# Performance work log

Measured on AMD Instinct MI355X. Metric: run time of the kernel, lower is better.

## Reference

```python
import jax, jax.numpy as jnp
import numpy as np

C, N = 3, 8192
FEATS = (64, 64, 1)
REG2, REG, REG_LENGTH = 1.0, 1.0, 4.0


def setup_inputs() -> dict:
    key = jax.random.key(0)
    k_x, k1, k2, k3 = jax.random.split(key, 4)
    x = jax.random.normal(k_x, (C, N), dtype=jnp.float32)
    # lecun_normal (flax Dense default): std = 1/sqrt(fan_in), no bias
    W1 = jax.random.normal(k1, (N, FEATS[0]), dtype=jnp.float32) / np.sqrt(N)
    W2 = jax.random.normal(k2, (FEATS[0], FEATS[1]), dtype=jnp.float32) / np.sqrt(FEATS[0])
    W3 = jax.random.normal(k3, (FEATS[1], FEATS[2]), dtype=jnp.float32) / np.sqrt(FEATS[1])
    regu2 = jnp.float32(REG2)
    regu = jnp.float32(REG)
    regu_length = jnp.float32(REG_LENGTH)
    return {"x": x, "W1": W1, "W2": W2, "W3": W3,
            "regu2": regu2, "regu": regu, "regu_length": regu_length}


def reference(x, W1, W2, W3, regu2, regu, regu_length):
    # x: (C, N)
    n = x.shape[1]
    # Circular cross-correlation rows: corr[i, j] = sum_c x[c, (i+j) % N] * x[c, i]
    corr = jax.vmap(
        lambda i: jnp.sum(jnp.roll(x, -i, axis=1) * x[:, i][:, None], axis=0)
    )(jnp.arange(n))  # (N, N)
    # tiny per-row MLP (Dense no-bias + elu), then sum over features
    z = jax.nn.elu(corr @ W1)
    z = jax.nn.elu(z @ W2)
    z = jax.nn.elu(z @ W3)
    per_row = jnp.sum(z, axis=-1)  # (N,)
    x2 = jnp.sum(x * x, axis=0)    # (N,)
    out = (jnp.mean(per_row)
           - regu2 * jnp.sum(x2)
           - regu * jnp.sum(jnp.exp(x2 / (2.0 * regu_length ** 2))))
    return out
```

## Files before the change

kernel.cpp:

```cpp
#include <hip/hip_runtime.h>
#include <hip/hip_bf16.h>

#define NN 8192
#define BM 32
#define BK 256
#define NT (NN / BK)
#define XWF 304

typedef short bfrag8 __attribute__((ext_vector_type(8)));
typedef float floatx4 __attribute__((ext_vector_type(4)));

static __device__ __forceinline__ unsigned short f2bf(float f) {
  unsigned u = __builtin_bit_cast(unsigned, f);
  u = (u + 0x7FFFu + ((u >> 16) & 1u)) >> 16;
  return (unsigned short)u;
}
static __device__ __forceinline__ unsigned cvt_pk_bf16(float a, float b) {
  return (unsigned)f2bf(a) | ((unsigned)f2bf(b) << 16);
}
static __device__ __forceinline__ float elu(float v) {
  return v > 0.f ? v : expm1f(v);
}

__global__ void prep_kernel(const float* __restrict__ x, const float* __restrict__ W1,
                            const float* __restrict__ W2, const float* __restrict__ rlen,
                            unsigned short* __restrict__ W1T, unsigned short* __restrict__ W2T,
                            float* __restrict__ acc) {
  const int b = blockIdx.x, t = threadIdx.x;
  if (b < 128) {
    __shared__ float tile[64][65];
    const int k0 = b * 64;
#pragma unroll
    for (int it = 0; it < 16; ++it) {
      int k = it * 4 + (t >> 6);
      tile[k][t & 63] = W1[(k0 + k) * 64 + (t & 63)];
    }
    __syncthreads();
#pragma unroll
    for (int it = 0; it < 16; ++it) {
      int f = it * 4 + (t >> 6);
      int kk = t & 63;
      W1T[f * NN + k0 + kk] = f2bf(tile[kk][f]);
    }
  } else if (b == 128) {
    for (int idx = t; idx < 64 * 64; idx += 256) {
      int k = idx >> 6, f = idx & 63;
      W2T[f * 64 + k] = f2bf(W2[idx]);
    }
  } else {
    float rl = rlen[0];
    float inv = 1.f / (2.f * rl * rl);
    int base = (b - 129) * 4096;
    float s1 = 0.f, s2 = 0.f;
    for (int ii = 0; ii < 16; ++ii) {
      int i = base + ii * 256 + t;
      float a0 = x[i], a1 = x[NN + i], a2 = x[2 * NN + i];
      float s = a0 * a0 + a1 * a1 + a2 * a2;
      s1 += s; s2 += expf(s * inv);
    }
    for (int d = 32; d > 0; d >>= 1) { s1 += __shfl_down(s1, d); s2 += __shfl_down(s2, d); }
    __shared__ float p1[4], p2[4];
    if ((t & 63) == 0) { p1[t >> 6] = s1; p2[t >> 6] = s2; }
    __syncthreads();
    if (t == 0) {
      atomicAdd(&acc[1], p1[0] + p1[1] + p1[2] + p1[3]);
      atomicAdd(&acc[2], p2[0] + p2[1] + p2[2] + p2[3]);
    }
  }
}

__global__ __launch_bounds__(512, 1) void main_kernel(
    const float* __restrict__ x, const unsigned short* __restrict__ W1T,
    const unsigned short* __restrict__ W2T, const float* __restrict__ W3,
    float* __restrict__ acc) {
  __shared__ __align__(16) unsigned short cr[2][BM * 256];
  __shared__ __align__(16) float xwinf[2][3][XWF];
  __shared__ float z3p[64];

  const int t = threadIdx.x;
  const int i0 = blockIdx.x * BM;
  const int wv = t >> 6;
  const int l = t & 63;
  const int lg = l >> 4, lr = l & 15;

  const int cg = l;
  const int sb = wv * 4 + cg * 4;

  const int np = wv & 1, quad = wv >> 1;
  const unsigned short* bp0 = W1T + (np * 32 + lr) * NN + quad * 32 + lg * 8;
  const unsigned short* bp1 = bp0 + 16 * NN;

  float xr[3][4];
#pragma unroll
  for (int c = 0; c < 3; ++c)
#pragma unroll
    for (int r = 0; r < 4; ++r)
      xr[c][r] = x[c * NN + i0 + wv * 4 + r];

  if (t < 216) {
    int c = t / 72, rr = t - c * 72;
    *(float4*)&xwinf[0][c][rr * 4] =
        *(const float4*)&x[c * NN + ((i0 + rr * 4) & (NN - 1))];
  }
  uint4 bA0 = *(const uint4*)(bp0);
  uint4 bA1 = *(const uint4*)(bp1);
  uint4 bB0 = *(const uint4*)(bp0 + 128);
  uint4 bB1 = *(const uint4*)(bp1 + 128);

  floatx4 acc00 = {0.f, 0.f, 0.f, 0.f}, acc01 = {0.f, 0.f, 0.f, 0.f};
  floatx4 acc10 = {0.f, 0.f, 0.f, 0.f}, acc11 = {0.f, 0.f, 0.f, 0.f};

  __syncthreads();

  for (int kt = 0; kt < NT; ++kt) {
    const int j0 = kt * BK;
    const int buf = kt & 1;
    const int jn = j0 + BK;
    const bool more = (kt + 1 < NT);

    float4 sv;
    int c_st = 0, rr_st = 0;
    const bool do_stage = more && (t < 216);
    if (do_stage) {
      c_st = t / 72; rr_st = t - c_st * 72;
      sv = *(const float4*)&x[c_st * NN + ((i0 + jn + rr_st * 4) & (NN - 1))];
    }
    uint4 nA0, nA1, nB0, nB1;
    if (more) {
      nA0 = *(const uint4*)(bp0 + jn);
      nA1 = *(const uint4*)(bp1 + jn);
      nB0 = *(const uint4*)(bp0 + jn + 128);
      nB1 = *(const uint4*)(bp1 + jn + 128);
    }

    float acf[4][4];
#pragma unroll
    for (int r = 0; r < 4; ++r)
#pragma unroll
      for (int j = 0; j < 4; ++j) acf[r][j] = 0.f;
#pragma unroll
    for (int c = 0; c < 3; ++c) {
      const float* wp = &xwinf[buf][c][sb];
      float4 v0 = *(const float4*)(wp);
      float4 v1 = *(const float4*)(wp + 4);
      float wf[7] = {v0.x, v0.y, v0.z, v0.w, v1.x, v1.y, v1.z};
#pragma unroll
      for (int r = 0; r < 4; ++r) {
        float xv = xr[c][r];
#pragma unroll
        for (int j = 0; j < 4; ++j) acf[r][j] = fmaf(xv, wf[r + j], acf[r][j]);
      }
    }
#pragma unroll
    for (int r = 0; r < 4; ++r) {
      const int row = wv * 4 + r;
      const int sw = ((cg >> 1) + 4 * row) & 31;
      unsigned u0 = cvt_pk_bf16(acf[r][0], acf[r][1]);
      unsigned u1 = cvt_pk_bf16(acf[r][2], acf[r][3]);
      uint2 q = {u0, u1};
      *(uint2*)((char*)&cr[buf][0] + row * 512 + sw * 16 + (cg & 1) * 8) = q;
    }
    if (do_stage) *(float4*)&xwinf[buf ^ 1][c_st][rr_st * 4] = sv;

    __syncthreads();

#pragma unroll
    for (int s2 = 0; s2 < 2; ++s2) {
      const int slot = (quad + s2 * 4) * 4 + lg;
      const int swz = (slot + 4 * lr) & 31;
      bfrag8 a0 = __builtin_bit_cast(bfrag8,
          *(const uint4*)((const char*)&cr[buf][0] + lr * 512 + swz * 16));
      bfrag8 a1 = __builtin_bit_cast(bfrag8,
          *(const uint4*)((const char*)&cr[buf][0] + (16 + lr) * 512 + swz * 16));
      bfrag8 b0 = __builtin_bit_cast(bfrag8, s2 == 0 ? bA0 : bB0);
      bfrag8 b1 = __builtin_bit_cast(bfrag8, s2 == 0 ? bA1 : bB1);
      acc00 = __builtin_amdgcn_mfma_f32_16x16x32_bf16(a0, b0, acc00, 0, 0, 0);
      acc01 = __builtin_amdgcn_mfma_f32_16x16x32_bf16(a0, b1, acc01, 0, 0, 0);
      acc10 = __builtin_amdgcn_mfma_f32_16x16x32_bf16(a1, b0, acc10, 0, 0, 0);
      acc11 = __builtin_amdgcn_mfma_f32_16x16x32_bf16(a1, b1, acc11, 0, 0, 0);
    }
    bA0 = nA0; bA1 = nA1; bB0 = nB0; bB1 = nB1;
  }

  float* h1buf = (float*)&cr[0][0];
  for (int q = t; q < 32 * 68; q += 512) h1buf[q] = 0.f;
  __syncthreads();
  {
#pragma unroll
    for (int m = 0; m < 2; ++m)
#pragma unroll
      for (int tn = 0; tn < 2; ++tn) {
        floatx4 a = (m == 0) ? (tn == 0 ? acc00 : acc01) : (tn == 0 ? acc10 : acc11);
#pragma unroll
        for (int r = 0; r < 4; ++r) {
          int row = m * 16 + lg * 4 + r;
          int col = np * 32 + tn * 16 + lr;
          atomicAdd(&h1buf[row * 68 + col], a[r]);
        }
      }
  }
  __syncthreads();

  if (t < 256) {
    const int w4 = t >> 6;
    const int m2 = w4 & 1, np2 = w4 >> 1;
    floatx4 acc2_0 = {0.f, 0.f, 0.f, 0.f}, acc2_1 = {0.f, 0.f, 0.f, 0.f};
#pragma unroll
    for (int ks2 = 0; ks2 < 2; ++ks2) {
      const int kb = ks2 * 32 + lg * 8;
      const float* hp = &h1buf[(m2 * 16 + lr) * 68 + kb];
      unsigned qa[4];
#pragma unroll
      for (int e = 0; e < 4; ++e) {
        float v0 = elu(hp[2 * e]), v1 = elu(hp[2 * e + 1]);
        qa[e] = cvt_pk_bf16(v0, v1);
      }
      uint4 qv = {qa[0], qa[1], qa[2], qa[3]};
      bfrag8 a2 = __builtin_bit_cast(bfrag8, qv);
#pragma unroll
      for (int tn = 0; tn < 2; ++tn) {
        int col2 = np2 * 32 + tn * 16 + lr;
        bfrag8 b2 = __builtin_bit_cast(bfrag8, *(const uint4*)&W2T[col2 * 64 + kb]);
        if (tn == 0)
          acc2_0 = __builtin_amdgcn_mfma_f32_16x16x32_bf16(a2, b2, acc2_0, 0, 0, 0);
        else
          acc2_1 = __builtin_amdgcn_mfma_f32_16x16x32_bf16(a2, b2, acc2_1, 0, 0, 0);
      }
    }
    float w3a = W3[np2 * 32 + lr];
    float w3b = W3[np2 * 32 + 16 + lr];
    float vsum[4];
#pragma unroll
    for (int r = 0; r < 4; ++r) {
      float v = elu(acc2_0[r]) * w3a + elu(acc2_1[r]) * w3b;
      v += __shfl_xor(v, 1); v += __shfl_xor(v, 2);
      v += __shfl_xor(v, 4); v += __shfl_xor(v, 8);
      vsum[r] = v;
    }
    if (lr == 0) {
#pragma unroll
      for (int r = 0; r < 4; ++r)
        z3p[(m2 * 16 + lg * 4 + r) * 2 + np2] = vsum[r];
    }
  }
  __syncthreads();
  if (t < 32) {
    float sv2 = z3p[t * 2] + z3p[t * 2 + 1];
    float z3 = elu(sv2);
    z3 += __shfl_xor(z3, 1); z3 += __shfl_xor(z3, 2); z3 += __shfl_xor(z3, 4);
    z3 += __shfl_xor(z3, 8); z3 += __shfl_xor(z3, 16);
    if (t == 0) atomicAdd(&acc[0], z3);
  }
}

__global__ void fin_kernel(const float* __restrict__ acc, const float* __restrict__ regu2,
                           const float* __restrict__ regu, float* __restrict__ out) {
  if (threadIdx.x == 0)
    out[0] = acc[0] * (1.f / (float)NN) - regu2[0] * acc[1] - regu[0] * acc[2];
}

extern "C" void kernel_launch(void* const* d_in, const int* in_sizes, int n_in,
                              void* d_out, int out_size, void* d_ws, size_t ws_size,
                              hipStream_t stream) {
  const float* x     = (const float*)d_in[0];
  const float* W1    = (const float*)d_in[1];
  const float* W2    = (const float*)d_in[2];
  const float* W3    = (const float*)d_in[3];
  const float* regu2 = (const float*)d_in[4];
  const float* regu  = (const float*)d_in[5];
  const float* rlen  = (const float*)d_in[6];

  char* ws = (char*)d_ws;
  float* acc            = (float*)ws;
  unsigned short* W1T   = (unsigned short*)(ws + 16);
  unsigned short* W2T   = (unsigned short*)(ws + 1048592);

  (void)hipMemsetAsync(acc, 0, 16, stream);
  prep_kernel<<<131, 256, 0, stream>>>(x, W1, W2, rlen, W1T, W2T, acc);
  main_kernel<<<256, 512, 0, stream>>>(x, W1T, W2T, W3, acc);
  fin_kernel<<<1, 64, 0, stream>>>(acc, regu2, regu, (float*)d_out);
}
```

Before: 120.3 us.

## Split K reduction across two blocks and move MLP tail to separate kernel

The main GEMM over the 8192-long correlation dimension is split in half so each row tile is handled by two blocks, doubling the grid from 256 to 512 blocks to fill more compute units. Partial first-layer results go to a global workspace, and a new tail kernel sums the halves and runs the second and third MLP layers. Bf16 packing of correlation values switches from round-to-nearest to truncation to save ALU work, and launch bounds allow more occupancy. This costs an extra kernel launch, about 4 MB of global traffic for partials, and slightly lower precision.

```diff
diff --git a/kernel.cpp b/kernel.cpp
--- a/kernel.cpp
+++ b/kernel.cpp
@@ -4,7 +4,6 @@
 #define NN 8192
 #define BM 32
 #define BK 256
-#define NT (NN / BK)
 #define XWF 304
 
 typedef short bfrag8 __attribute__((ext_vector_type(8)));
@@ -17,6 +16,11 @@
 }
 static __device__ __forceinline__ unsigned cvt_pk_bf16(float a, float b) {
   return (unsigned)f2bf(a) | ((unsigned)f2bf(b) << 16);
+}
+static __device__ __forceinline__ unsigned trunc_pk_bf16(float a, float b) {
+  unsigned ua = __builtin_bit_cast(unsigned, a);
+  unsigned ub = __builtin_bit_cast(unsigned, b);
+  return (ub & 0xFFFF0000u) | (ua >> 16);
 }
 static __device__ __forceinline__ float elu(float v) {
   return v > 0.f ? v : expm1f(v);
@@ -69,16 +73,17 @@
   }
 }
 
-__global__ __launch_bounds__(512, 1) void main_kernel(
+__global__ __launch_bounds__(512, 4) void main_kernel(
     const float* __restrict__ x, const unsigned short* __restrict__ W1T,
-    const unsigned short* __restrict__ W2T, const float* __restrict__ W3,
-    float* __restrict__ acc) {
+    float* __restrict__ part) {
   __shared__ __align__(16) unsigned short cr[2][BM * 256];
   __shared__ __align__(16) float xwinf[2][3][XWF];
-  __shared__ float z3p[64];
 
   const int t = threadIdx.x;
-  const int i0 = blockIdx.x * BM;
+  const int ib = blockIdx.x >> 1;
+  const int hb = blockIdx.x & 1;
+  const int i0 = ib * BM;
+  const int kt0 = hb * 16;
   const int wv = t >> 6;
   const int l = t & 63;
   const int lg = l >> 4, lr = l & 15;
@@ -89,6 +94,7 @@
   const int np = wv & 1, quad = wv >> 1;
   const unsigned short* bp0 = W1T + (np * 32 + lr) * NN + quad * 32 + lg * 8;
   const unsigned short* bp1 = bp0 + 16 * NN;
+  const int koff0 = kt0 * BK;
 
   float xr[3][4];
 #pragma unroll
@@ -100,23 +106,22 @@
   if (t < 216) {
     int c = t / 72, rr = t - c * 72;
     *(float4*)&xwinf[0][c][rr * 4] =
-        *(const float4*)&x[c * NN + ((i0 + rr * 4) & (NN - 1))];
-  }
-  uint4 bA0 = *(const uint4*)(bp0);
-  uint4 bA1 = *(const uint4*)(bp1);
-  uint4 bB0 = *(const uint4*)(bp0 + 128);
-  uint4 bB1 = *(const uint4*)(bp1 + 128);
+        *(const float4*)&x[c * NN + ((i0 + koff0 + rr * 4) & (NN - 1))];
+  }
+  uint4 bA0 = *(const uint4*)(bp0 + koff0);
+  uint4 bA1 = *(const uint4*)(bp1 + koff0);
+  uint4 bB0 = *(const uint4*)(bp0 + koff0 + 128);
+  uint4 bB1 = *(const uint4*)(bp1 + koff0 + 128);
 
   floatx4 acc00 = {0.f, 0.f, 0.f, 0.f}, acc01 = {0.f, 0.f, 0.f, 0.f};
   floatx4 acc10 = {0.f, 0.f, 0.f, 0.f}, acc11 = {0.f, 0.f, 0.f, 0.f};
 
   __syncthreads();
 
-  for (int kt = 0; kt < NT; ++kt) {
-    const int j0 = kt * BK;
-    const int buf = kt & 1;
-    const int jn = j0 + BK;
-    const bool more = (kt + 1 < NT);
+  for (int ktt = 0; ktt < 16; ++ktt) {
+    const int buf = ktt & 1;
+    const int jn = (kt0 + ktt + 1) * BK;
+    const bool more = (ktt + 1 < 16);
 
     float4 sv;
     int c_st = 0, rr_st = 0;
@@ -155,8 +160,8 @@
     for (int r = 0; r < 4; ++r) {
       const int row = wv * 4 + r;
       const int sw = ((cg >> 1) + 4 * row) & 31;
-      unsigned u0 = cvt_pk_bf16(acf[r][0], acf[r][1]);
-      unsigned u1 = cvt_pk_bf16(acf[r][2], acf[r][3]);
+      unsigned u0 = trunc_pk_bf16(acf[r][0], acf[r][1]);
+      unsigned u1 = trunc_pk_bf16(acf[r][2], acf[r][3]);
       uint2 q = {u0, u1};
       *(uint2*)((char*)&cr[buf][0] + row * 512 + sw * 16 + (cg & 1) * 8) = q;
     }
@@ -201,18 +206,41 @@
   }
   __syncthreads();
 
-  if (t < 256) {
-    const int w4 = t >> 6;
-    const int m2 = w4 & 1, np2 = w4 >> 1;
+  for (int q = t; q < BM * 64; q += 512) {
+    int row = q >> 6, col = q & 63;
+    part[hb * (NN * 64) + (i0 + row) * 64 + col] = h1buf[row * 68 + col];
+  }
+}
+
+__global__ __launch_bounds__(256, 4) void tail_kernel(
+    const float* __restrict__ part, const unsigned short* __restrict__ W2T,
+    const float* __restrict__ W3, float* __restrict__ acc) {
+  __shared__ float z3p[256];
+  __shared__ float bsum[2];
+  const int t = threadIdx.x;
+  const int w4 = t >> 6, l = t & 63;
+  const int lg = l >> 4, lr = l & 15;
+  const int m2 = w4 & 1, np2 = w4 >> 1;
+  const int i0 = blockIdx.x * 128;
+
+  const float w3a = W3[np2 * 32 + lr];
+  const float w3b = W3[np2 * 32 + 16 + lr];
+
+#pragma unroll
+  for (int rg = 0; rg < 4; ++rg) {
+    const int rbase = i0 + rg * 32;
     floatx4 acc2_0 = {0.f, 0.f, 0.f, 0.f}, acc2_1 = {0.f, 0.f, 0.f, 0.f};
 #pragma unroll
     for (int ks2 = 0; ks2 < 2; ++ks2) {
       const int kb = ks2 * 32 + lg * 8;
-      const float* hp = &h1buf[(m2 * 16 + lr) * 68 + kb];
+      const int row = rbase + m2 * 16 + lr;
+      const float* p0 = &part[row * 64 + kb];
+      const float* p1 = &part[NN * 64 + row * 64 + kb];
       unsigned qa[4];
 #pragma unroll
       for (int e = 0; e < 4; ++e) {
-        float v0 = elu(hp[2 * e]), v1 = elu(hp[2 * e + 1]);
+        float v0 = elu(p0[2 * e] + p1[2 * e]);
+        float v1 = elu(p0[2 * e + 1] + p1[2 * e + 1]);
         qa[e] = cvt_pk_bf16(v0, v1);
       }
       uint4 qv = {qa[0], qa[1], qa[2], qa[3]};
@@ -227,30 +255,25 @@
           acc2_1 = __builtin_amdgcn_mfma_f32_16x16x32_bf16(a2, b2, acc2_1, 0, 0, 0);
       }
     }
-    float w3a = W3[np2 * 32 + lr];
-    float w3b = W3[np2 * 32 + 16 + lr];
-    float vsum[4];
 #pragma unroll
     for (int r = 0; r < 4; ++r) {
       float v = elu(acc2_0[r]) * w3a + elu(acc2_1[r]) * w3b;
       v += __shfl_xor(v, 1); v += __shfl_xor(v, 2);
       v += __shfl_xor(v, 4); v += __shfl_xor(v, 8);
-      vsum[r] = v;
-    }
-    if (lr == 0) {
-#pragma unroll
-      for (int r = 0; r < 4; ++r)
-        z3p[(m2 * 16 + lg * 4 + r) * 2 + np2] = vsum[r];
-    }
-  }
-  __syncthreads();
-  if (t < 32) {
+      if (lr == 0)
+        z3p[(rg * 32 + m2 * 16 + lg * 4 + r) * 2 + np2] = v;
+    }
+  }
+  __syncthreads();
+  if (t < 128) {
     float sv2 = z3p[t * 2] + z3p[t * 2 + 1];
     float z3 = elu(sv2);
     z3 += __shfl_xor(z3, 1); z3 += __shfl_xor(z3, 2); z3 += __shfl_xor(z3, 4);
-    z3 += __shfl_xor(z3, 8); z3 += __shfl_xor(z3, 16);
-    if (t == 0) atomicAdd(&acc[0], z3);
-  }
+    z3 += __shfl_xor(z3, 8); z3 += __shfl_xor(z3, 16); z3 += __shfl_xor(z3, 32);
+    if ((t & 63) == 0) bsum[t >> 6] = z3;
+  }
+  __syncthreads();
+  if (t == 0) atomicAdd(&acc[0], bsum[0] + bsum[1]);
 }
 
 __global__ void fin_kernel(const float* __restrict__ acc, const float* __restrict__ regu2,
@@ -274,9 +297,11 @@
   float* acc            = (float*)ws;
   unsigned short* W1T   = (unsigned short*)(ws + 16);
   unsigned short* W2T   = (unsigned short*)(ws + 1048592);
+  float* part           = (float*)(ws + 1056784);
 
   (void)hipMemsetAsync(acc, 0, 16, stream);
   prep_kernel<<<131, 256, 0, stream>>>(x, W1, W2, rlen, W1T, W2T, acc);
-  main_kernel<<<256, 512, 0, stream>>>(x, W1T, W2T, W3, acc);
+  main_kernel<<<512, 512, 0, stream>>>(x, W1T, part);
+  tail_kernel<<<64, 256, 0, stream>>>(part, W2T, W3, acc);
   fin_kernel<<<1, 64, 0, stream>>>(acc, regu2, regu, (float*)d_out);
 }
```

Result: slower. 150.7 us (+25.3%).
